# Kernel optimization log

Measured on AMD Instinct MI355X. Metric: run time of the kernel, lower is better.

Reference implementation:

```python
import jax, jax.numpy as jnp
import numpy as np

N_NODES = 100000
N_EDGES = 1000000
DIM_IN = 64
DIM_H = 64
DIM_OUT = 1


def _lin_init(key, out_dim, in_dim):
    # torch Linear default: U(-1/sqrt(fan_in), 1/sqrt(fan_in))
    bound = 1.0 / np.sqrt(in_dim)
    return jax.random.uniform(key, (out_dim, in_dim), jnp.float32, -bound, bound)


def setup_inputs() -> dict:
    key = jax.random.key(0)
    ks = jax.random.split(key, 10)
    x = jax.random.normal(ks[0], (N_NODES, DIM_IN), jnp.float32)
    edge_index = jax.random.randint(ks[1], (2, N_EDGES), 0, N_NODES, dtype=jnp.int64)
    # layer 0: SAGEConv(DIM_IN, DIM_H): lin_l (with bias) on aggregated neighbors, lin_r (no bias) on root
    Wl0 = _lin_init(ks[2], DIM_H, DIM_IN)
    bl0 = jax.random.uniform(ks[3], (DIM_H,), jnp.float32, -1.0 / np.sqrt(DIM_IN), 1.0 / np.sqrt(DIM_IN))
    Wr0 = _lin_init(ks[4], DIM_H, DIM_IN)
    # layer 1: SAGEConv(DIM_H, DIM_OUT)
    Wl1 = _lin_init(ks[5], DIM_OUT, DIM_H)
    bl1 = jax.random.uniform(ks[6], (DIM_OUT,), jnp.float32, -1.0 / np.sqrt(DIM_H), 1.0 / np.sqrt(DIM_H))
    Wr1 = _lin_init(ks[7], DIM_OUT, DIM_H)
    return {"x": x, "edge_index": edge_index,
            "Wl0": Wl0, "bl0": bl0, "Wr0": Wr0,
            "Wl1": Wl1, "bl1": bl1, "Wr1": Wr1}


def sage_conv(h, src, dst, Wl, bl, Wr):
    # messages: gather source-node features per edge, mean-aggregate into destination nodes
    msg = h[src]                                                   # [E, d]
    summed = jax.ops.segment_sum(msg, dst, num_segments=N_NODES)   # [N, d]
    deg = jax.ops.segment_sum(jnp.ones((src.shape[0],), h.dtype), dst, num_segments=N_NODES)
    mean_nb = summed / jnp.maximum(deg, 1.0)[:, None]
    # out = lin_l(mean_neighbors) + lin_r(x_root)
    return mean_nb @ Wl.T + bl + h @ Wr.T


def reference(x, edge_index, Wl0, bl0, Wr0, Wl1, bl1, Wr1):
    src, dst = edge_index[0], edge_index[1]
    h = sage_conv(x, src, dst, Wl0, bl0, Wr0)
    h = jax.nn.relu(h)  # dropout is identity in eval mode
    h = sage_conv(h, src, dst, Wl1, bl1, Wr1)
    return (h, jax.nn.sigmoid(h))
```

## Files before the change

kernel.cpp:

```cpp
#include <hip/hip_runtime.h>
#include <hip/hip_bf16.h>
#include <math.h>

#define N_NODES 100000
#define N_EDGES 1000000
#define DIM 64
#define SCAN_BLOCKS 391
#define AGPAD 72
#define NHB 125
#define HTHREADS 1024
#define EPB (N_EDGES / NHB)
#define HWORDS ((N_NODES + 3) / 4)

typedef __hip_bfloat16 bf16;
typedef __attribute__((ext_vector_type(8))) short short8;
typedef __attribute__((ext_vector_type(4))) float floatx4;

__device__ __forceinline__ float b2f(bf16 v) { return __bfloat162float(v); }

__device__ __forceinline__ unsigned int packbf2(float a, float b) {
    bf16 x = __float2bfloat16(a), y = __float2bfloat16(b);
    unsigned short ux = *(unsigned short*)&x, uy = *(unsigned short*)&y;
    return (unsigned int)ux | ((unsigned int)uy << 16);
}

__device__ __forceinline__ short f2bs(float v) {
    bf16 x = __float2bfloat16(v);
    return *(short*)&x;
}

__device__ __forceinline__ float2 upk(unsigned int u) {
    unsigned short lo = (unsigned short)(u & 0xffff);
    unsigned short hi = (unsigned short)(u >> 16);
    bf16 a = *(bf16*)&lo, b = *(bf16*)&hi;
    return make_float2(b2f(a), b2f(b));
}

__device__ __forceinline__ int clampN(int v) {
    return v < 0 ? 0 : (v >= N_NODES ? N_NODES - 1 : v);
}


__global__ __launch_bounds__(HTHREADS) void count_kernel(const int* __restrict__ ei,
                                                         unsigned int* __restrict__ bh32) {
    __shared__ unsigned int cnt[HWORDS];
    const int t = threadIdx.x, b = blockIdx.x;
    for (int w = t; w < HWORDS; w += HTHREADS) cnt[w] = 0u;
    __syncthreads();
    const int4* dst4 = (const int4*)(ei + N_EDGES + b * EPB);
    for (int k = t; k < EPB / 4; k += HTHREADS) {
        int4 d4 = dst4[k];
        int d;
        d = clampN(d4.x); atomicAdd(&cnt[d >> 2], 1u << (8 * (d & 3)));
        d = clampN(d4.y); atomicAdd(&cnt[d >> 2], 1u << (8 * (d & 3)));
        d = clampN(d4.z); atomicAdd(&cnt[d >> 2], 1u << (8 * (d & 3)));
        d = clampN(d4.w); atomicAdd(&cnt[d >> 2], 1u << (8 * (d & 3)));
    }
    __syncthreads();
    unsigned int* out = bh32 + (long)b * HWORDS;
    for (int w = t; w < HWORDS; w += HTHREADS) out[w] = cnt[w];
}

__global__ void convert_kernel(const float4* __restrict__ x4,
                               uint2* __restrict__ xb4,
                               const float* __restrict__ Wl0,
                               const float* __restrict__ Wr0,
                               short* __restrict__ wt) {
    int b = blockIdx.x;
    if (b < 6250) {
        int idx = b * 256 + threadIdx.x;
        float4 f = x4[idx];
        xb4[idx] = make_uint2(packbf2(f.x, f.y), packbf2(f.z, f.w));
    } else {
        for (int i = threadIdx.x; i < 8192; i += 256) {
            int d = i >> 7, k = i & 127;
            float v = (k < 64) ? Wl0[d * 64 + k] : Wr0[d * 64 + (k - 64)];
            wt[i] = f2bs(v);
        }
    }
}

__global__ void scan1_kernel(unsigned char* __restrict__ bhb,
                             int* __restrict__ degi,
                             int* __restrict__ rowstart, int* __restrict__ bsum) {
    __shared__ int sc[256];
    int t = threadIdx.x;
    int i = blockIdx.x * 256 + t;
    int v = 0;
    if (i < N_NODES) {
        int sum = 0;
        #pragma unroll 5
        for (int c = 0; c < NHB; ++c) {
            long off = (long)c * (HWORDS * 4) + i;
            int u = bhb[off];
            bhb[off] = (unsigned char)sum;
            sum += u;
        }
        degi[i] = sum;
        v = sum;
    }
    sc[t] = v;
    __syncthreads();
    #pragma unroll
    for (int off = 1; off < 256; off <<= 1) {
        int u = (t >= off) ? sc[t - off] : 0;
        __syncthreads();
        sc[t] += u;
        __syncthreads();
    }
    if (i < N_NODES) rowstart[i] = sc[t] - v;
    if (t == 255) bsum[blockIdx.x] = sc[t];
}

__global__ void scan2_kernel(int* __restrict__ bsum) {
    __shared__ int sc[512];
    int t = threadIdx.x;
    int v = (t < SCAN_BLOCKS) ? bsum[t] : 0;
    sc[t] = v;
    __syncthreads();
    #pragma unroll
    for (int off = 1; off < 512; off <<= 1) {
        int u = (t >= off) ? sc[t - off] : 0;
        __syncthreads();
        sc[t] += u;
        __syncthreads();
    }
    if (t < SCAN_BLOCKS) bsum[t] = sc[t] - v;
}

__global__ __launch_bounds__(HTHREADS) void fill_kernel(const int* __restrict__ ei,
                                                        const int* __restrict__ rowstart,
                                                        const int* __restrict__ bsum,
                                                        const unsigned int* __restrict__ bh32,
                                                        int* __restrict__ csr) {
    __shared__ unsigned int cnt[HWORDS];
    const int t = threadIdx.x, b = blockIdx.x;
    const unsigned int* in = bh32 + (long)b * HWORDS;
    for (int w = t; w < HWORDS; w += HTHREADS) cnt[w] = in[w];
    __syncthreads();
    const int4* srcp4 = (const int4*)(ei + b * EPB);
    const int4* dstp4 = (const int4*)(ei + N_EDGES + b * EPB);
    for (int k = t; k < EPB / 4; k += HTHREADS) {
        int4 s4 = srcp4[k];
        int4 d4 = dstp4[k];
        int d, sv;
        unsigned int old;
        d = clampN(d4.x); sv = clampN(s4.x);
        old = atomicAdd(&cnt[d >> 2], 1u << (8 * (d & 3)));
        csr[rowstart[d] + bsum[d >> 8] + (int)((old >> (8 * (d & 3))) & 0xffu)] = sv;
        d = clampN(d4.y); sv = clampN(s4.y);
        old = atomicAdd(&cnt[d >> 2], 1u << (8 * (d & 3)));
        csr[rowstart[d] + bsum[d >> 8] + (int)((old >> (8 * (d & 3))) & 0xffu)] = sv;
        d = clampN(d4.z); sv = clampN(s4.z);
        old = atomicAdd(&cnt[d >> 2], 1u << (8 * (d & 3)));
        csr[rowstart[d] + bsum[d >> 8] + (int)((old >> (8 * (d & 3))) & 0xffu)] = sv;
        d = clampN(d4.w); sv = clampN(s4.w);
        old = atomicAdd(&cnt[d >> 2], 1u << (8 * (d & 3)));
        csr[rowstart[d] + bsum[d >> 8] + (int)((old >> (8 * (d & 3))) & 0xffu)] = sv;
    }
}

__global__ __launch_bounds__(256) void agg_gemm_kernel(
        const uint2* __restrict__ xb2, const short* __restrict__ xb,
        const short* __restrict__ wt,
        const int* __restrict__ rowstart, const int* __restrict__ bsum,
        const int* __restrict__ degi, const int* __restrict__ csr,
        const float* __restrict__ bl0, const float* __restrict__ Wl1,
        const float* __restrict__ Wr1,
        float* __restrict__ s, float* __restrict__ t) {
    __shared__ short As[16 * AGPAD];
    __shared__ float sRed[16], tRed[16];
    const int tid = threadIdx.x;
    const int nb = blockIdx.x * 16;

    if (tid < 16) { sRed[tid] = 0.0f; tRed[tid] = 0.0f; }

    {
        int qn = tid >> 4;
        int l  = tid & 15;
        int n = nb + qn;
        int beg = rowstart[n] + bsum[n >> 8];
        int cnt = degi[n];
        float4 A0 = make_float4(0.f, 0.f, 0.f, 0.f);
        float4 A1 = A0, A2 = A0, A3 = A0;
        int i = 0;
        if (cnt >= 8) {
            const int* cp = csr + beg;
            int e0 = cp[0], e1 = cp[1], e2 = cp[2], e3 = cp[3];
            int e4 = cp[4], e5 = cp[5], e6 = cp[6], e7 = cp[7];
            for (;;) {
                uint2 u0 = xb2[(long)e0 * 16 + l];
                uint2 u1 = xb2[(long)e1 * 16 + l];
                uint2 u2 = xb2[(long)e2 * 16 + l];
                uint2 u3 = xb2[(long)e3 * 16 + l];
                uint2 u4 = xb2[(long)e4 * 16 + l];
                uint2 u5 = xb2[(long)e5 * 16 + l];
                uint2 u6 = xb2[(long)e6 * 16 + l];
                uint2 u7 = xb2[(long)e7 * 16 + l];
                int ni = i + 8;
                bool more = (ni + 8 <= cnt);
                int f0, f1, f2, f3, f4, f5, f6, f7;
                if (more) {
                    const int* np = csr + beg + ni;
                    f0 = np[0]; f1 = np[1]; f2 = np[2]; f3 = np[3];
                    f4 = np[4]; f5 = np[5]; f6 = np[6]; f7 = np[7];
                }
                float2 f;
                f = upk(u0.x); A0.x += f.x; A0.y += f.y; f = upk(u0.y); A0.z += f.x; A0.w += f.y;
                f = upk(u1.x); A1.x += f.x; A1.y += f.y; f = upk(u1.y); A1.z += f.x; A1.w += f.y;
                f = upk(u2.x); A2.x += f.x; A2.y += f.y; f = upk(u2.y); A2.z += f.x; A2.w += f.y;
                f = upk(u3.x); A3.x += f.x; A3.y += f.y; f = upk(u3.y); A3.z += f.x; A3.w += f.y;
                f = upk(u4.x); A0.x += f.x; A0.y += f.y; f = upk(u4.y); A0.z += f.x; A0.w += f.y;
                f = upk(u5.x); A1.x += f.x; A1.y += f.y; f = upk(u5.y); A1.z += f.x; A1.w += f.y;
                f = upk(u6.x); A2.x += f.x; A2.y += f.y; f = upk(u6.y); A2.z += f.x; A2.w += f.y;
                f = upk(u7.x); A3.x += f.x; A3.y += f.y; f = upk(u7.y); A3.z += f.x; A3.w += f.y;
                i = ni;
                if (!more) break;
                e0 = f0; e1 = f1; e2 = f2; e3 = f3;
                e4 = f4; e5 = f5; e6 = f6; e7 = f7;
            }
        }
        if (i + 4 <= cnt) {
            int e0 = csr[beg + i],     e1 = csr[beg + i + 1];
            int e2 = csr[beg + i + 2], e3 = csr[beg + i + 3];
            uint2 u0 = xb2[(long)e0 * 16 + l];
            uint2 u1 = xb2[(long)e1 * 16 + l];
            uint2 u2 = xb2[(long)e2 * 16 + l];
            uint2 u3 = xb2[(long)e3 * 16 + l];
            float2 f;
            f = upk(u0.x); A0.x += f.x; A0.y += f.y; f = upk(u0.y); A0.z += f.x; A0.w += f.y;
            f = upk(u1.x); A1.x += f.x; A1.y += f.y; f = upk(u1.y); A1.z += f.x; A1.w += f.y;
            f = upk(u2.x); A2.x += f.x; A2.y += f.y; f = upk(u2.y); A2.z += f.x; A2.w += f.y;
            f = upk(u3.x); A3.x += f.x; A3.y += f.y; f = upk(u3.y); A3.z += f.x; A3.w += f.y;
            i += 4;
        }
        if (i < cnt) {
            uint2 u = xb2[(long)csr[beg + i] * 16 + l];
            float2 f = upk(u.x); A0.x += f.x; A0.y += f.y;
            f = upk(u.y); A0.z += f.x; A0.w += f.y;
        }
        if (i + 1 < cnt) {
            uint2 u = xb2[(long)csr[beg + i + 1] * 16 + l];
            float2 f = upk(u.x); A1.x += f.x; A1.y += f.y;
            f = upk(u.y); A1.z += f.x; A1.w += f.y;
        }
        if (i + 2 < cnt) {
            uint2 u = xb2[(long)csr[beg + i + 2] * 16 + l];
            float2 f = upk(u.x); A2.x += f.x; A2.y += f.y;
            f = upk(u.y); A2.z += f.x; A2.w += f.y;
        }
        float inv = 1.0f / fmaxf((float)cnt, 1.0f);
        float ax = (A0.x + A1.x + A2.x + A3.x) * inv;
        float ay = (A0.y + A1.y + A2.y + A3.y) * inv;
        float az = (A0.z + A1.z + A2.z + A3.z) * inv;
        float aw = (A0.w + A1.w + A2.w + A3.w) * inv;
        *(uint2*)&As[qn * AGPAD + 4 * l] =
            make_uint2(packbf2(ax, ay), packbf2(az, aw));
    }
    __syncthreads();

    const int lane = tid & 63;
    const int w = tid >> 6;
    const int r = lane & 15;
    const int quad = lane >> 4;

    short8 a0 = *(const short8*)&As[r * AGPAD + quad * 8];
    short8 a1 = *(const short8*)&As[r * AGPAD + 32 + quad * 8];
    const long xrow = (long)(nb + r) * 64 + quad * 8;
    short8 a2 = *(const short8*)(xb + xrow);
    short8 a3 = *(const short8*)(xb + xrow + 32);

    const int d = w * 16 + r;
    const short* brow = wt + (long)d * 128 + quad * 8;
    short8 b0 = *(const short8*)(brow);
    short8 b1 = *(const short8*)(brow + 32);
    short8 b2 = *(const short8*)(brow + 64);
    short8 b3 = *(const short8*)(brow + 96);

    float bb = bl0[d];
    floatx4 acc = {bb, bb, bb, bb};
    acc = __builtin_amdgcn_mfma_f32_16x16x32_bf16(a0, b0, acc, 0, 0, 0);
    acc = __builtin_amdgcn_mfma_f32_16x16x32_bf16(a1, b1, acc, 0, 0, 0);
    acc = __builtin_amdgcn_mfma_f32_16x16x32_bf16(a2, b2, acc, 0, 0, 0);
    acc = __builtin_amdgcn_mfma_f32_16x16x32_bf16(a3, b3, acc, 0, 0, 0);

    float w1 = Wl1[d], w2 = Wr1[d];
    float hs[4], ht[4];
    #pragma unroll
    for (int g = 0; g < 4; ++g) {
        float h = fmaxf(acc[g], 0.0f);
        hs[g] = h * w1;
        ht[g] = h * w2;
    }
    #pragma unroll
    for (int g = 0; g < 4; ++g) {
        #pragma unroll
        for (int off = 1; off < 16; off <<= 1) {
            hs[g] += __shfl_xor(hs[g], off, 64);
            ht[g] += __shfl_xor(ht[g], off, 64);
        }
    }
    if (r == 0) {
        #pragma unroll
        for (int g = 0; g < 4; ++g) {
            atomicAdd(&sRed[quad * 4 + g], hs[g]);
            atomicAdd(&tRed[quad * 4 + g], ht[g]);
        }
    }
    __syncthreads();
    if (tid < 16) {
        s[nb + tid] = sRed[tid];
        t[nb + tid] = tRed[tid];
    }
}

__global__ void final_kernel(const float* __restrict__ s,
                             const float* __restrict__ t,
                             const int* __restrict__ rowstart,
                             const int* __restrict__ bsum,
                             const int* __restrict__ degi,
                             const int* __restrict__ csr,
                             const float* __restrict__ bl1,
                             float* __restrict__ out) {
    int n = blockIdx.x * 256 + threadIdx.x;
    if (n >= N_NODES) return;
    int beg = rowstart[n] + bsum[n >> 8];
    int cnt = degi[n];
    float acc = 0.0f;
    int i = 0;
    for (; i + 4 <= cnt; i += 4) {
        int e0 = csr[beg + i], e1 = csr[beg + i + 1];
        int e2 = csr[beg + i + 2], e3 = csr[beg + i + 3];
        acc += s[e0] + s[e1] + s[e2] + s[e3];
    }
    for (; i < cnt; ++i) acc += s[csr[beg + i]];
    float v = acc / fmaxf((float)cnt, 1.0f) + bl1[0] + t[n];
    float sg = 1.0f / (1.0f + expf(-v));
    out[n] = v;
    out[N_NODES + n] = sg;
}

extern "C" void kernel_launch(void* const* d_in, const int* in_sizes, int n_in,
                              void* d_out, int out_size, void* d_ws, size_t ws_size,
                              hipStream_t stream) {
    const float* x   = (const float*)d_in[0];
    const int*   ei  = (const int*)d_in[1];
    const float* Wl0 = (const float*)d_in[2];
    const float* bl0 = (const float*)d_in[3];
    const float* Wr0 = (const float*)d_in[4];
    const float* Wl1 = (const float*)d_in[5];
    const float* bl1 = (const float*)d_in[6];
    const float* Wr1 = (const float*)d_in[7];
    float* out = (float*)d_out;

    char* ws = (char*)d_ws;
    int*   degi     = (int*)(ws);
    int*   rowstart = (int*)(ws + 400000);
    int*   bsum     = (int*)(ws + 800000);
    float* s        = (float*)(ws + 804096);
    float* t        = (float*)(ws + 1204096);
    int*   csr      = (int*)(ws + 1604096);
    char*  xb       = (ws + 5604096);
    short* wt       = (short*)(ws + 18404096);
    char*  bh       = (ws + 18420480);

    count_kernel<<<NHB, HTHREADS, 0, stream>>>(ei, (unsigned int*)bh);
    convert_kernel<<<6251, 256, 0, stream>>>((const float4*)x, (uint2*)xb,
                                             Wl0, Wr0, wt);
    scan1_kernel<<<SCAN_BLOCKS, 256, 0, stream>>>((unsigned char*)bh, degi,
                                                  rowstart, bsum);
    scan2_kernel<<<1, 512, 0, stream>>>(bsum);
    fill_kernel<<<NHB, HTHREADS, 0, stream>>>(ei, rowstart, bsum,
                                              (const unsigned int*)bh, csr);
    agg_gemm_kernel<<<6250, 256, 0, stream>>>((const uint2*)xb, (const short*)xb,
                                              wt, rowstart, bsum, degi, csr,
                                              bl0, Wl1, Wr1, s, t);
    final_kernel<<<SCAN_BLOCKS, 256, 0, stream>>>(s, t, rowstart, bsum, degi, csr,
                                                  bl1, out);
}
```

Measured before the change: 181.2 us.

## Sort nodes by in-degree to balance aggregation work across warps

Builds a degree histogram during the scan, prefix-sums it, and creates a permutation of nodes grouped by in-degree (clamped at 63). The aggregation GEMM and final kernels process nodes in this permuted order, so the 16 nodes in a block and the threads of a wave have similar neighbor counts, which reduces divergence and tail imbalance. In exchange it adds a memset, an extra kernel, indirect node indexing, and scattered rather than contiguous reads of root features and writes of s/t/out.

```diff
diff --git a/kernel.cpp b/kernel.cpp
--- a/kernel.cpp
+++ b/kernel.cpp
@@ -82,10 +82,14 @@
 
 __global__ void scan1_kernel(unsigned char* __restrict__ bhb,
                              int* __restrict__ degi,
-                             int* __restrict__ rowstart, int* __restrict__ bsum) {
+                             int* __restrict__ rowstart, int* __restrict__ bsum,
+                             int* __restrict__ dhist) {
     __shared__ int sc[256];
+    __shared__ int dh[64];
     int t = threadIdx.x;
     int i = blockIdx.x * 256 + t;
+    if (t < 64) dh[t] = 0;
+    __syncthreads();
     int v = 0;
     if (i < N_NODES) {
         int sum = 0;
@@ -98,6 +102,7 @@
         }
         degi[i] = sum;
         v = sum;
+        atomicAdd(&dh[v < 63 ? v : 63], 1);
     }
     sc[t] = v;
     __syncthreads();
@@ -110,9 +115,10 @@
     }
     if (i < N_NODES) rowstart[i] = sc[t] - v;
     if (t == 255) bsum[blockIdx.x] = sc[t];
-}
-
-__global__ void scan2_kernel(int* __restrict__ bsum) {
+    if (t < 64 && dh[t] > 0) atomicAdd(&dhist[t], dh[t]);
+}
+
+__global__ void scan2_kernel(int* __restrict__ bsum, int* __restrict__ dhist) {
     __shared__ int sc[512];
     int t = threadIdx.x;
     int v = (t < SCAN_BLOCKS) ? bsum[t] : 0;
@@ -126,6 +132,32 @@
         __syncthreads();
     }
     if (t < SCAN_BLOCKS) bsum[t] = sc[t] - v;
+    if (t == 0) {
+        int run = 0;
+        #pragma unroll
+        for (int k = 0; k < 64; ++k) { int u = dhist[k]; dhist[k] = run; run += u; }
+    }
+}
+
+__global__ void perm_kernel(const int* __restrict__ degi,
+                            int* __restrict__ dbase,
+                            int* __restrict__ perm) {
+    __shared__ unsigned int c64[64];
+    __shared__ int g64[64];
+    int t = threadIdx.x;
+    int n = blockIdx.x * 256 + t;
+    if (t < 64) c64[t] = 0u;
+    __syncthreads();
+    int bin = 0; unsigned int rank = 0; bool valid = (n < N_NODES);
+    if (valid) {
+        int dg = degi[n];
+        bin = dg < 63 ? dg : 63;
+        rank = atomicAdd(&c64[bin], 1u);
+    }
+    __syncthreads();
+    if (t < 64) { unsigned int c = c64[t]; g64[t] = c ? atomicAdd(&dbase[t], (int)c) : 0; }
+    __syncthreads();
+    if (valid) perm[g64[bin] + (int)rank] = n;
 }
 
 __global__ __launch_bounds__(HTHREADS) void fill_kernel(const int* __restrict__ ei,
@@ -165,20 +197,26 @@
         const short* __restrict__ wt,
         const int* __restrict__ rowstart, const int* __restrict__ bsum,
         const int* __restrict__ degi, const int* __restrict__ csr,
+        const int* __restrict__ perm,
         const float* __restrict__ bl0, const float* __restrict__ Wl1,
         const float* __restrict__ Wr1,
         float* __restrict__ s, float* __restrict__ t) {
     __shared__ short As[16 * AGPAD];
     __shared__ float sRed[16], tRed[16];
+    __shared__ int nid[16];
     const int tid = threadIdx.x;
     const int nb = blockIdx.x * 16;
 
-    if (tid < 16) { sRed[tid] = 0.0f; tRed[tid] = 0.0f; }
+    if (tid < 16) {
+        sRed[tid] = 0.0f; tRed[tid] = 0.0f;
+        nid[tid] = perm[nb + tid];
+    }
+    __syncthreads();
 
     {
         int qn = tid >> 4;
         int l  = tid & 15;
-        int n = nb + qn;
+        int n = nid[qn];
         int beg = rowstart[n] + bsum[n >> 8];
         int cnt = degi[n];
         float4 A0 = make_float4(0.f, 0.f, 0.f, 0.f);
@@ -266,7 +304,7 @@
 
     short8 a0 = *(const short8*)&As[r * AGPAD + quad * 8];
     short8 a1 = *(const short8*)&As[r * AGPAD + 32 + quad * 8];
-    const long xrow = (long)(nb + r) * 64 + quad * 8;
+    const long xrow = (long)nid[r] * 64 + quad * 8;
     short8 a2 = *(const short8*)(xb + xrow);
     short8 a3 = *(const short8*)(xb + xrow + 32);
 
@@ -309,8 +347,8 @@
     }
     __syncthreads();
     if (tid < 16) {
-        s[nb + tid] = sRed[tid];
-        t[nb + tid] = tRed[tid];
+        s[nid[tid]] = sRed[tid];
+        t[nid[tid]] = tRed[tid];
     }
 }
 
@@ -320,10 +358,12 @@
                              const int* __restrict__ bsum,
                              const int* __restrict__ degi,
                              const int* __restrict__ csr,
+                             const int* __restrict__ perm,
                              const float* __restrict__ bl1,
                              float* __restrict__ out) {
-    int n = blockIdx.x * 256 + threadIdx.x;
-    if (n >= N_NODES) return;
+    int idx = blockIdx.x * 256 + threadIdx.x;
+    if (idx >= N_NODES) return;
+    int n = perm[idx];
     int beg = rowstart[n] + bsum[n >> 8];
     int cnt = degi[n];
     float acc = 0.0f;
@@ -363,18 +403,23 @@
     char*  xb       = (ws + 5604096);
     short* wt       = (short*)(ws + 18404096);
     char*  bh       = (ws + 18420480);
+    int*   perm     = (int*)(ws + 30920480);
+    int*   dhist    = (int*)(ws + 31320480);
+
+    (void)hipMemsetAsync(dhist, 0, 256, stream);
 
     count_kernel<<<NHB, HTHREADS, 0, stream>>>(ei, (unsigned int*)bh);
     convert_kernel<<<6251, 256, 0, stream>>>((const float4*)x, (uint2*)xb,
                                              Wl0, Wr0, wt);
     scan1_kernel<<<SCAN_BLOCKS, 256, 0, stream>>>((unsigned char*)bh, degi,
-                                                  rowstart, bsum);
-    scan2_kernel<<<1, 512, 0, stream>>>(bsum);
+                                                  rowstart, bsum, dhist);
+    scan2_kernel<<<1, 512, 0, stream>>>(bsum, dhist);
+    perm_kernel<<<SCAN_BLOCKS, 256, 0, stream>>>(degi, dhist, perm);
     fill_kernel<<<NHB, HTHREADS, 0, stream>>>(ei, rowstart, bsum,
                                               (const unsigned int*)bh, csr);
     agg_gemm_kernel<<<6250, 256, 0, stream>>>((const uint2*)xb, (const short*)xb,
-                                              wt, rowstart, bsum, degi, csr,
+                                              wt, rowstart, bsum, degi, csr, perm,
                                               bl0, Wl1, Wr1, s, t);
     final_kernel<<<SCAN_BLOCKS, 256, 0, stream>>>(s, t, rowstart, bsum, degi, csr,
-                                                  bl1, out);
-}
+                                                  perm, bl1, out);
+}
```

After: 195.3 us. 1.08x slower.

## Split histogram kernels by node halves and fuse conversion into scan

Applied to the files above, without the earlier changes.

Count and fill kernels now launch two blocks per edge segment, each keeping only half of the node histogram in shared memory (50KB instead of 100KB). This allows more blocks per CU and doubles the grid from 125 to 250 blocks on a large GPU. The cost is that each block reads its whole edge segment and filters out edges outside its half. Separately, the bf16 conversion of x and the weights is merged into the scan1 launch to remove one kernel launch.

```diff
diff --git a/kernel.cpp b/kernel.cpp
--- a/kernel.cpp
+++ b/kernel.cpp
@@ -11,6 +11,8 @@
 #define HTHREADS 1024
 #define EPB (N_EDGES / NHB)
 #define HWORDS ((N_NODES + 3) / 4)
+#define HALF_NODES (N_NODES / 2)
+#define HWORDS_HALF (HALF_NODES / 4)
 
 typedef __hip_bfloat16 bf16;
 typedef __attribute__((ext_vector_type(8))) short short8;
@@ -43,49 +45,54 @@
 
 __global__ __launch_bounds__(HTHREADS) void count_kernel(const int* __restrict__ ei,
                                                          unsigned int* __restrict__ bh32) {
-    __shared__ unsigned int cnt[HWORDS];
-    const int t = threadIdx.x, b = blockIdx.x;
-    for (int w = t; w < HWORDS; w += HTHREADS) cnt[w] = 0u;
-    __syncthreads();
-    const int4* dst4 = (const int4*)(ei + N_EDGES + b * EPB);
+    __shared__ unsigned int cnt[HWORDS_HALF];
+    const int t = threadIdx.x;
+    const int seg = blockIdx.x >> 1, half = blockIdx.x & 1;
+    const int nlo = half * HALF_NODES, nhi = nlo + HALF_NODES;
+    for (int w = t; w < HWORDS_HALF; w += HTHREADS) cnt[w] = 0u;
+    __syncthreads();
+    const int4* dst4 = (const int4*)(ei + N_EDGES + seg * EPB);
     for (int k = t; k < EPB / 4; k += HTHREADS) {
         int4 d4 = dst4[k];
         int d;
-        d = clampN(d4.x); atomicAdd(&cnt[d >> 2], 1u << (8 * (d & 3)));
-        d = clampN(d4.y); atomicAdd(&cnt[d >> 2], 1u << (8 * (d & 3)));
-        d = clampN(d4.z); atomicAdd(&cnt[d >> 2], 1u << (8 * (d & 3)));
-        d = clampN(d4.w); atomicAdd(&cnt[d >> 2], 1u << (8 * (d & 3)));
-    }
-    __syncthreads();
-    unsigned int* out = bh32 + (long)b * HWORDS;
-    for (int w = t; w < HWORDS; w += HTHREADS) out[w] = cnt[w];
-}
-
-__global__ void convert_kernel(const float4* __restrict__ x4,
-                               uint2* __restrict__ xb4,
-                               const float* __restrict__ Wl0,
-                               const float* __restrict__ Wr0,
-                               short* __restrict__ wt) {
+        d = clampN(d4.x); if (d >= nlo && d < nhi) { int ld = d - nlo; atomicAdd(&cnt[ld >> 2], 1u << (8 * (ld & 3))); }
+        d = clampN(d4.y); if (d >= nlo && d < nhi) { int ld = d - nlo; atomicAdd(&cnt[ld >> 2], 1u << (8 * (ld & 3))); }
+        d = clampN(d4.z); if (d >= nlo && d < nhi) { int ld = d - nlo; atomicAdd(&cnt[ld >> 2], 1u << (8 * (ld & 3))); }
+        d = clampN(d4.w); if (d >= nlo && d < nhi) { int ld = d - nlo; atomicAdd(&cnt[ld >> 2], 1u << (8 * (ld & 3))); }
+    }
+    __syncthreads();
+    unsigned int* out = bh32 + (long)seg * HWORDS + half * HWORDS_HALF;
+    for (int w = t; w < HWORDS_HALF; w += HTHREADS) out[w] = cnt[w];
+}
+
+__global__ void scan1_convert_kernel(unsigned char* __restrict__ bhb,
+                                     int* __restrict__ degi,
+                                     int* __restrict__ rowstart,
+                                     int* __restrict__ bsum,
+                                     const float4* __restrict__ x4,
+                                     uint2* __restrict__ xb4,
+                                     const float* __restrict__ Wl0,
+                                     const float* __restrict__ Wr0,
+                                     short* __restrict__ wt) {
+    __shared__ int sc[256];
     int b = blockIdx.x;
-    if (b < 6250) {
-        int idx = b * 256 + threadIdx.x;
-        float4 f = x4[idx];
-        xb4[idx] = make_uint2(packbf2(f.x, f.y), packbf2(f.z, f.w));
-    } else {
-        for (int i = threadIdx.x; i < 8192; i += 256) {
-            int d = i >> 7, k = i & 127;
-            float v = (k < 64) ? Wl0[d * 64 + k] : Wr0[d * 64 + (k - 64)];
-            wt[i] = f2bs(v);
-        }
-    }
-}
-
-__global__ void scan1_kernel(unsigned char* __restrict__ bhb,
-                             int* __restrict__ degi,
-                             int* __restrict__ rowstart, int* __restrict__ bsum) {
-    __shared__ int sc[256];
     int t = threadIdx.x;
-    int i = blockIdx.x * 256 + t;
+    if (b >= SCAN_BLOCKS) {
+        int bb = b - SCAN_BLOCKS;
+        if (bb < 6250) {
+            int idx = bb * 256 + t;
+            float4 f = x4[idx];
+            xb4[idx] = make_uint2(packbf2(f.x, f.y), packbf2(f.z, f.w));
+        } else {
+            for (int i = t; i < 8192; i += 256) {
+                int d = i >> 7, k = i & 127;
+                float v = (k < 64) ? Wl0[d * 64 + k] : Wr0[d * 64 + (k - 64)];
+                wt[i] = f2bs(v);
+            }
+        }
+        return;
+    }
+    int i = b * 256 + t;
     int v = 0;
     if (i < N_NODES) {
         int sum = 0;
@@ -109,7 +116,7 @@
         __syncthreads();
     }
     if (i < N_NODES) rowstart[i] = sc[t] - v;
-    if (t == 255) bsum[blockIdx.x] = sc[t];
+    if (t == 255) bsum[b] = sc[t];
 }
 
 __global__ void scan2_kernel(int* __restrict__ bsum) {
@@ -133,30 +140,44 @@
                                                         const int* __restrict__ bsum,
                                                         const unsigned int* __restrict__ bh32,
                                                         int* __restrict__ csr) {
-    __shared__ unsigned int cnt[HWORDS];
-    const int t = threadIdx.x, b = blockIdx.x;
-    const unsigned int* in = bh32 + (long)b * HWORDS;
-    for (int w = t; w < HWORDS; w += HTHREADS) cnt[w] = in[w];
-    __syncthreads();
-    const int4* srcp4 = (const int4*)(ei + b * EPB);
-    const int4* dstp4 = (const int4*)(ei + N_EDGES + b * EPB);
+    __shared__ unsigned int cnt[HWORDS_HALF];
+    const int t = threadIdx.x;
+    const int seg = blockIdx.x >> 1, half = blockIdx.x & 1;
+    const int nlo = half * HALF_NODES, nhi = nlo + HALF_NODES;
+    const unsigned int* in = bh32 + (long)seg * HWORDS + half * HWORDS_HALF;
+    for (int w = t; w < HWORDS_HALF; w += HTHREADS) cnt[w] = in[w];
+    __syncthreads();
+    const int4* srcp4 = (const int4*)(ei + seg * EPB);
+    const int4* dstp4 = (const int4*)(ei + N_EDGES + seg * EPB);
     for (int k = t; k < EPB / 4; k += HTHREADS) {
         int4 s4 = srcp4[k];
         int4 d4 = dstp4[k];
-        int d, sv;
+        int d, ld, sv;
         unsigned int old;
-        d = clampN(d4.x); sv = clampN(s4.x);
-        old = atomicAdd(&cnt[d >> 2], 1u << (8 * (d & 3)));
-        csr[rowstart[d] + bsum[d >> 8] + (int)((old >> (8 * (d & 3))) & 0xffu)] = sv;
-        d = clampN(d4.y); sv = clampN(s4.y);
-        old = atomicAdd(&cnt[d >> 2], 1u << (8 * (d & 3)));
-        csr[rowstart[d] + bsum[d >> 8] + (int)((old >> (8 * (d & 3))) & 0xffu)] = sv;
-        d = clampN(d4.z); sv = clampN(s4.z);
-        old = atomicAdd(&cnt[d >> 2], 1u << (8 * (d & 3)));
-        csr[rowstart[d] + bsum[d >> 8] + (int)((old >> (8 * (d & 3))) & 0xffu)] = sv;
-        d = clampN(d4.w); sv = clampN(s4.w);
-        old = atomicAdd(&cnt[d >> 2], 1u << (8 * (d & 3)));
-        csr[rowstart[d] + bsum[d >> 8] + (int)((old >> (8 * (d & 3))) & 0xffu)] = sv;
+        d = clampN(d4.x);
+        if (d >= nlo && d < nhi) {
+            ld = d - nlo; sv = clampN(s4.x);
+            old = atomicAdd(&cnt[ld >> 2], 1u << (8 * (ld & 3)));
+            csr[rowstart[d] + bsum[d >> 8] + (int)((old >> (8 * (ld & 3))) & 0xffu)] = sv;
+        }
+        d = clampN(d4.y);
+        if (d >= nlo && d < nhi) {
+            ld = d - nlo; sv = clampN(s4.y);
+            old = atomicAdd(&cnt[ld >> 2], 1u << (8 * (ld & 3)));
+            csr[rowstart[d] + bsum[d >> 8] + (int)((old >> (8 * (ld & 3))) & 0xffu)] = sv;
+        }
+        d = clampN(d4.z);
+        if (d >= nlo && d < nhi) {
+            ld = d - nlo; sv = clampN(s4.z);
+            old = atomicAdd(&cnt[ld >> 2], 1u << (8 * (ld & 3)));
+            csr[rowstart[d] + bsum[d >> 8] + (int)((old >> (8 * (ld & 3))) & 0xffu)] = sv;
+        }
+        d = clampN(d4.w);
+        if (d >= nlo && d < nhi) {
+            ld = d - nlo; sv = clampN(s4.w);
+            old = atomicAdd(&cnt[ld >> 2], 1u << (8 * (ld & 3)));
+            csr[rowstart[d] + bsum[d >> 8] + (int)((old >> (8 * (ld & 3))) & 0xffu)] = sv;
+        }
     }
 }
 
@@ -364,14 +385,13 @@
     short* wt       = (short*)(ws + 18404096);
     char*  bh       = (ws + 18420480);
 
-    count_kernel<<<NHB, HTHREADS, 0, stream>>>(ei, (unsigned int*)bh);
-    convert_kernel<<<6251, 256, 0, stream>>>((const float4*)x, (uint2*)xb,
-                                             Wl0, Wr0, wt);
-    scan1_kernel<<<SCAN_BLOCKS, 256, 0, stream>>>((unsigned char*)bh, degi,
-                                                  rowstart, bsum);
+    count_kernel<<<2 * NHB, HTHREADS, 0, stream>>>(ei, (unsigned int*)bh);
+    scan1_convert_kernel<<<SCAN_BLOCKS + 6251, 256, 0, stream>>>(
+        (unsigned char*)bh, degi, rowstart, bsum,
+        (const float4*)x, (uint2*)xb, Wl0, Wr0, wt);
     scan2_kernel<<<1, 512, 0, stream>>>(bsum);
-    fill_kernel<<<NHB, HTHREADS, 0, stream>>>(ei, rowstart, bsum,
-                                              (const unsigned int*)bh, csr);
+    fill_kernel<<<2 * NHB, HTHREADS, 0, stream>>>(ei, rowstart, bsum,
+                                                  (const unsigned int*)bh, csr);
     agg_gemm_kernel<<<6250, 256, 0, stream>>>((const uint2*)xb, (const short*)xb,
                                               wt, rowstart, bsum, degi, csr,
                                               bl0, Wl1, Wr1, s, t);
```

New measurement: 170.9 us. 5.7% less time.
